# Performance work log

Hardware: AMD Instinct MI355X
Metric: run time of the kernel (lower is better)

The kernel has to match this reference:

```python
import jax, jax.numpy as jnp
import numpy as np

NUM_CODES = 1024
CODE_DIM = 256
COMMIT_W = 0.25
EPS = 1e-5
ENT_LO, ENT_HI = 0.5, 0.9
ENT_W = 0.1
VAR_FLOOR = 0.05
VAR_W = 1e-3
DECORR_W = 1e-3


def setup_inputs() -> dict:
    key = jax.random.key(0)
    k1, k2, k3 = jax.random.split(key, 3)
    inputs = jax.random.normal(k1, (16, 2048, CODE_DIM), dtype=jnp.float32)
    weight = jax.random.normal(k2, (NUM_CODES, CODE_DIM), dtype=jnp.float32) * 0.1
    usage_counts = jax.random.uniform(k3, (NUM_CODES,), dtype=jnp.float32)
    return {"inputs": inputs, "weight": weight, "usage_counts": usage_counts}


def reference(inputs, weight, usage_counts):
    K, D = weight.shape
    flat = inputs.reshape(-1, D)  # [N, D]
    # squared euclidean distances [N, K]
    dist = (flat ** 2).sum(axis=1, keepdims=True) - 2.0 * flat @ weight.T + (weight ** 2).sum(axis=1)
    idx = jnp.argmin(dist, axis=1)  # [N]
    quant = weight[idx].reshape(inputs.shape)

    commitment_loss = COMMIT_W * jnp.mean((jax.lax.stop_gradient(quant) - inputs) ** 2)
    # straight-through estimator
    quant_ste = inputs + jax.lax.stop_gradient(quant - inputs)

    # usage entropy regularizer
    probs = usage_counts + EPS
    probs = probs / jnp.maximum(probs.sum(), EPS * K)
    usage_entropy = -jnp.sum(probs * jnp.log(probs + EPS)) / np.log(float(K)).astype(np.float32)
    gap = jnp.where(usage_entropy < ENT_LO, ENT_LO - usage_entropy,
                    jnp.where(usage_entropy > ENT_HI, usage_entropy - ENT_HI, 0.0))
    entropy_loss = ENT_W * gap ** 2

    # variance floor penalty on codebook
    variance = jnp.var(weight, axis=0)
    variance_loss = VAR_W * jnp.mean(jax.nn.relu(VAR_FLOOR - variance))

    # decorrelation penalty
    wc = weight - weight.mean(axis=0, keepdims=True)
    cov = wc.T @ wc / float(K)  # [D, D]
    off_diag = cov - jnp.diag(jnp.diag(cov))
    decorrelation_loss = DECORR_W * jnp.mean(off_diag ** 2)

    total_loss = commitment_loss + entropy_loss + variance_loss + decorrelation_loss
    indices = idx.reshape(inputs.shape[:-1])
    return (quant_ste, indices, total_loss, commitment_loss, entropy_loss,
            variance_loss, decorrelation_loss, usage_entropy)
```

## Files before the change

kernel.cpp:

```cpp
#include <hip/hip_runtime.h>
#include <math.h>

#define DIMS   256
#define KCODES 1024
#define NTOT   32768
#define TAU    4.0e-4f

typedef __bf16 bf16x8 __attribute__((ext_vector_type(8)));
typedef float  f32x4  __attribute__((ext_vector_type(4)));

#define WS_COMMIT   0
#define WS_FLAGCNT  1
#define WS_DECORR   2
#define WS_COLSUM   16
#define WS_COLSQ    272
#define WS_WSQ      1024
#define WS_XSQ      2048
#define WS_FLAGS    34816
#define WS_CAND1    67584
#define WS_CAND2    329728
#define WS_CANDI    591872
#define WS_WP       854016

#define OUT_Q    0
#define OUT_IDX  8388608
#define OUT_SCAL 8421376


__global__ __launch_bounds__(256) void prep_kernel(const float* __restrict__ X,
                                                   const float* __restrict__ W,
                                                   __bf16* __restrict__ Xp,
                                                   __bf16* __restrict__ Wp2,
                                                   float* ws) {
  int b = blockIdx.x;
  int tid = threadIdx.x;
  if (b < 1056) {
    bool isW = b >= 1024;
    const float* src = isW ? W : X;
    __bf16* dst = isW ? Wp2 : Xp;
    int sqoff = isW ? WS_WSQ : WS_XSQ;
    int bb = isW ? b - 1024 : b;
    int kt = tid >> 5, mtl = (tid >> 4) & 1, lc = tid & 15;
    int row = bb * 32 + mtl * 16 + lc;
    int bt = row >> 7, c = row & 127;
    int wv = c >> 6, t = (c >> 4) & 3;
    size_t hibase = ((((size_t)(bt * 8 + kt) * 2 + wv) * 4 + t) * 2) * 512;
    const float* s = src + (size_t)row * DIMS + kt * 32;
    float sq = 0.f;
    #pragma unroll
    for (int kq = 0; kq < 4; kq++) {
      float4 u = *(const float4*)(s + kq * 8);
      float4 v = *(const float4*)(s + kq * 8 + 4);
      float f[8] = {u.x, u.y, u.z, u.w, v.x, v.y, v.z, v.w};
      bf16x8 hi, lo;
      #pragma unroll
      for (int e = 0; e < 8; e++) {
        __bf16 h = (__bf16)f[e];
        hi[e] = h;
        lo[e] = (__bf16)(f[e] - (float)h);
        sq = fmaf(f[e], f[e], sq);
      }
      size_t off = (size_t)(kq * 16 + lc) * 8;
      *(bf16x8*)&dst[hibase + off] = hi;
      *(bf16x8*)&dst[hibase + 512 + off] = lo;
    }
    atomicAdd(&ws[sqoff + row], sq);
  } else if (b < 1064) {
    int d = tid;
    int r0 = (b - 1056) * 128;
    float s = 0.f, sq = 0.f;
    #pragma unroll 8
    for (int k = 0; k < 128; k++) {
      float v = W[(size_t)(r0 + k) * DIMS + d];
      s += v;
      sq = fmaf(v, v, sq);
    }
    atomicAdd(&ws[WS_COLSUM + d], s);
    atomicAdd(&ws[WS_COLSQ + d], sq);
  } else {
    __shared__ float wi_s[2][KCODES];
    __shared__ float red2[256];
    __shared__ float mi_s[2];
    __shared__ float red[4];
    int i0 = (b - 1064) * 2;
    int rr = tid >> 1, cc = tid & 1;
    #pragma unroll
    for (int q = 0; q < 8; q++) {
      int row = q * 128 + rr;
      wi_s[cc][row] = W[(size_t)row * DIMS + i0 + cc];
    }
    __syncthreads();
    float pm = 0.f;
    #pragma unroll
    for (int q = 0; q < 8; q++) pm += wi_s[cc][rr * 8 + q];
    red2[tid] = pm;
    __syncthreads();
    if (tid < 2) {
      float s = 0.f;
      for (int k = tid; k < 256; k += 2) s += red2[k];
      mi_s[tid] = s * (1.0f / 1024.0f);
    }
    int j = tid;
    float a0 = 0.f, a1 = 0.f, sj = 0.f;
    for (int k = 0; k < KCODES; k += 4) {
      #pragma unroll
      for (int u = 0; u < 4; u++) {
        float wj = W[(size_t)(k + u) * DIMS + j];
        a0 = fmaf(wi_s[0][k + u], wj, a0);
        a1 = fmaf(wi_s[1][k + u], wj, a1);
        sj += wj;
      }
    }
    __syncthreads();
    const float inv = 1.0f / 1024.0f;
    float mj = sj * inv;
    float v = 0.f;
    float c0 = a0 * inv - mi_s[0] * mj;
    if (i0 != j) v = fmaf(c0, c0, v);
    float c1 = a1 * inv - mi_s[1] * mj;
    if (i0 + 1 != j) v = fmaf(c1, c1, v);
    #pragma unroll
    for (int m = 32; m >= 1; m >>= 1) v += __shfl_xor(v, m);
    if ((j & 63) == 0) red[j >> 6] = v;
    __syncthreads();
    if (j == 0) atomicAdd(&ws[WS_DECORR], (red[0] + red[1]) + (red[2] + red[3]));
  }
}

__global__ __launch_bounds__(256, 2) void pass1_kernel(const __bf16* __restrict__ Xp,
                                                       const __bf16* __restrict__ Wp2,
                                                       float* ws) {
  __shared__ float wsqs[128];
  __shared__ float d1L[256];
  __shared__ float d2L[256];
  __shared__ int   i1L[256];

  int tid = threadIdx.x;
  int lane = tid & 63, wave = tid >> 6;
  int wm = wave >> 1, wn = wave & 1;
  int quad = lane >> 4, col = lane & 15;
  int l = blockIdx.x;
  int bm = (l & 7) * 32 + ((l >> 3) & 31);
  int bn = l >> 8;
  int rowBase = bm * 128, cb = bn * 128;

  if (tid < 128) wsqs[tid] = ws[WS_WSQ + cb + tid];

  f32x4 acc[4][4];
  #pragma unroll
  for (int i = 0; i < 4; i++)
    #pragma unroll
    for (int j = 0; j < 4; j++) acc[i][j] = (f32x4){0.f, 0.f, 0.f, 0.f};

  const bf16x8* ab = (const bf16x8*)(Xp + (size_t)bm * 65536 + wm * 4096) + lane;
  const bf16x8* bb = (const bf16x8*)(Wp2 + (size_t)bn * 65536 + wn * 4096) + lane;

  bf16x8 Af[2][8], Bf[2][8];
  #pragma unroll
  for (int f = 0; f < 4; f++) {
    Af[0][f * 2] = ab[f * 128];
    Af[0][f * 2 + 1] = ab[f * 128 + 64];
    Bf[0][f * 2] = bb[f * 128];
    Bf[0][f * 2 + 1] = bb[f * 128 + 64];
  }
  #pragma unroll
  for (int kt = 0; kt < 8; kt++) {
    const int cur = kt & 1, nxt = cur ^ 1;
    if (kt < 7) {
      const bf16x8* an = ab + (kt + 1) * 1024;
      const bf16x8* bv = bb + (kt + 1) * 1024;
      #pragma unroll
      for (int f = 0; f < 4; f++) {
        Af[nxt][f * 2] = an[f * 128];
        Af[nxt][f * 2 + 1] = an[f * 128 + 64];
        Bf[nxt][f * 2] = bv[f * 128];
        Bf[nxt][f * 2 + 1] = bv[f * 128 + 64];
      }
    }
    #pragma unroll
    for (int nt = 0; nt < 4; nt++) {
      #pragma unroll
      for (int mt = 0; mt < 4; mt++) {
        acc[mt][nt] = __builtin_amdgcn_mfma_f32_16x16x32_bf16(Af[cur][mt * 2], Bf[cur][nt * 2], acc[mt][nt], 0, 0, 0);
        acc[mt][nt] = __builtin_amdgcn_mfma_f32_16x16x32_bf16(Af[cur][mt * 2], Bf[cur][nt * 2 + 1], acc[mt][nt], 0, 0, 0);
        acc[mt][nt] = __builtin_amdgcn_mfma_f32_16x16x32_bf16(Af[cur][mt * 2 + 1], Bf[cur][nt * 2], acc[mt][nt], 0, 0, 0);
      }
    }
  }
  __syncthreads();

  #pragma unroll
  for (int mt = 0; mt < 4; mt++) {
    #pragma unroll
    for (int r = 0; r < 4; r++) {
      float d1 = 3.0e38f, d2 = 3.0e38f;
      int i1 = 0;
      #pragma unroll
      for (int nt = 0; nt < 4; nt++) {
        int lc = wn * 64 + nt * 16 + col;
        float d = wsqs[lc] - 2.0f * acc[mt][nt][r];
        int g = cb + lc;
        if (d < d1) { d2 = d1; d1 = d; i1 = g; }
        else if (d < d2) d2 = d;
      }
      #pragma unroll
      for (int m = 1; m < 16; m <<= 1) {
        float od1 = __shfl_xor(d1, m);
        int oi1 = __shfl_xor(i1, m);
        float od2 = __shfl_xor(d2, m);
        if (od1 < d1 || (od1 == d1 && oi1 < i1)) {
          d2 = fminf(d1, fminf(d2, od2));
          d1 = od1; i1 = oi1;
        } else {
          d2 = fminf(od1, fminf(d2, od2));
        }
      }
      if (col == 0) {
        int lr = wm * 64 + mt * 16 + quad * 4 + r;
        d1L[lr * 2 + wn] = d1;
        d2L[lr * 2 + wn] = d2;
        i1L[lr * 2 + wn] = i1;
      }
    }
  }
  __syncthreads();
  if (tid < 128) {
    float a1 = d1L[tid * 2], a2 = d2L[tid * 2];
    int ai = i1L[tid * 2];
    float b1 = d1L[tid * 2 + 1], b2 = d2L[tid * 2 + 1];
    int bi = i1L[tid * 2 + 1];
    float m1, m2; int mi;
    if (b1 < a1 || (b1 == a1 && bi < ai)) { m1 = b1; mi = bi; m2 = fminf(a1, b2); }
    else { m1 = a1; mi = ai; m2 = fminf(b1, a2); }
    int o = bn * NTOT + rowBase + tid;
    ws[WS_CAND1 + o] = m1;
    ws[WS_CAND2 + o] = m2;
    ((int*)ws)[WS_CANDI + o] = mi;
  }
}

__global__ __launch_bounds__(256) void pass2_kernel(const float* __restrict__ W,
                                                    float* __restrict__ outQ,
                                                    float* __restrict__ outIdx, float* ws) {
  __shared__ int idx_s[256];
  int tid = threadIdx.x;
  int row = blockIdx.x * 256 + tid;
  const float* c1 = ws + WS_CAND1;
  const float* c2 = ws + WS_CAND2;
  const int* ci = (const int*)ws + WS_CANDI;
  float m1 = 3.0e38f, m2 = 3.0e38f;
  int mi = 0;
  #pragma unroll
  for (int b = 0; b < 8; b++) {
    int o = b * NTOT + row;
    float b1 = c1[o], b2 = c2[o];
    int bi = ci[o];
    if (b1 < m1 || (b1 == m1 && bi < mi)) { m2 = fminf(m1, b2); m1 = b1; mi = bi; }
    else { m2 = fminf(m2, b1); }
  }
  outIdx[row] = (float)mi;
  idx_s[tid] = mi;
  int* wsI = (int*)ws;
  if (m2 - m1 < TAU) {
    int p = atomicAdd(&wsI[WS_FLAGCNT], 1);
    wsI[WS_FLAGS + p] = row;
  }
  float partial = ws[WS_XSQ + row] + m1;
  #pragma unroll
  for (int m = 32; m >= 1; m >>= 1) partial += __shfl_xor(partial, m);
  if ((tid & 63) == 0) atomicAdd(&ws[WS_COMMIT], partial);
  __syncthreads();
  int wave = tid >> 6, lane = tid & 63;
  int rowBase = blockIdx.x * 256;
  #pragma unroll 4
  for (int i = 0; i < 64; i++) {
    int rl = wave * 64 + i;
    int ix = idx_s[rl];
    float4 v = ((const float4*)(W + (size_t)ix * DIMS))[lane];
    ((float4*)(outQ + (size_t)(rowBase + rl) * DIMS))[lane] = v;
  }
}

__global__ __launch_bounds__(256) void refine_kernel(const float* __restrict__ X,
                                                     const float* __restrict__ W,
                                                     float* __restrict__ outQ,
                                                     float* __restrict__ outIdx, float* ws,
                                                     const float* __restrict__ U,
                                                     float* __restrict__ out) {
  __shared__ float xs[DIMS];
  __shared__ double dm[256];
  __shared__ int im[256];
  __shared__ int chosen;
  int tid = threadIdx.x;
  if (blockIdx.x == 512) {
    __shared__ float red[256];
    float s = 0.f;
    for (int e = tid; e < KCODES; e += 256) s += U[e] + 1e-5f;
    red[tid] = s;
    __syncthreads();
    for (int st = 128; st >= 1; st >>= 1) {
      if (tid < st) red[tid] += red[tid + st];
      __syncthreads();
    }
    float S = red[0];
    __syncthreads();
    float denom = fmaxf(S, 1e-5f * 1024.0f);
    float h = 0.f;
    for (int e = tid; e < KCODES; e += 256) {
      float p = (U[e] + 1e-5f) / denom;
      h += p * logf(p + 1e-5f);
    }
    red[tid] = h;
    __syncthreads();
    for (int st = 128; st >= 1; st >>= 1) {
      if (tid < st) red[tid] += red[tid + st];
      __syncthreads();
    }
    float H = -red[0] / 6.93147180559945f;
    __syncthreads();
    float m = ws[WS_COLSUM + tid] * (1.0f / 1024.0f);
    float var = ws[WS_COLSQ + tid] * (1.0f / 1024.0f) - m * m;
    float r = 0.05f - var;
    red[tid] = r > 0.f ? r : 0.f;
    __syncthreads();
    for (int st = 128; st >= 1; st >>= 1) {
      if (tid < st) red[tid] += red[tid + st];
      __syncthreads();
    }
    if (tid == 0) {
      float varloss = 1e-3f * (red[0] / 256.0f);
      float gap = H < 0.5f ? (0.5f - H) : (H > 0.9f ? (H - 0.9f) : 0.0f);
      float entloss = 0.1f * gap * gap;
      float commit = 0.25f * ws[WS_COMMIT] / 8388608.0f;
      float dec = 1e-3f * ws[WS_DECORR] / 65536.0f;
      float* sc = out + OUT_SCAL;
      sc[0] = commit + entloss + varloss + dec;
      sc[1] = commit;
      sc[2] = entloss;
      sc[3] = varloss;
      sc[4] = dec;
      sc[5] = H;
    }
    return;
  }
  const int* wsI = (const int*)ws;
  int cnt = wsI[WS_FLAGCNT];
  const int* list = wsI + WS_FLAGS;
  for (int f = blockIdx.x; f < cnt; f += 512) {
    int row = list[f];
    __syncthreads();
    if (tid < 64) ((float4*)xs)[tid] = ((const float4*)(X + (size_t)row * DIMS))[tid];
    __syncthreads();
    double bd = 1.0e300;
    int bi = 0;
    for (int jj = 0; jj < 4; jj++) {
      int c = tid + 256 * jj;
      double a0 = 0.0, a1 = 0.0, a2 = 0.0, a3 = 0.0;
      const float* wr = W + (size_t)c * DIMS;
      #pragma unroll 4
      for (int d4 = 0; d4 < 64; d4++) {
        float4 w = ((const float4*)wr)[d4];
        float4 x = ((const float4*)xs)[d4];
        double e0 = (double)x.x - (double)w.x;
        double e1 = (double)x.y - (double)w.y;
        double e2 = (double)x.z - (double)w.z;
        double e3 = (double)x.w - (double)w.w;
        a0 += e0 * e0; a1 += e1 * e1; a2 += e2 * e2; a3 += e3 * e3;
      }
      double s = (a0 + a1) + (a2 + a3);
      if (s < bd) { bd = s; bi = c; }
    }
    dm[tid] = bd; im[tid] = bi;
    __syncthreads();
    for (int st = 128; st >= 1; st >>= 1) {
      if (tid < st) {
        if (dm[tid + st] < dm[tid] || (dm[tid + st] == dm[tid] && im[tid + st] < im[tid])) {
          dm[tid] = dm[tid + st]; im[tid] = im[tid + st];
        }
      }
      __syncthreads();
    }
    if (tid == 0) { chosen = im[0]; outIdx[row] = (float)im[0]; }
    __syncthreads();
    int ix = chosen;
    if (tid < 64)
      ((float4*)(outQ + (size_t)row * DIMS))[tid] = ((const float4*)(W + (size_t)ix * DIMS))[tid];
  }
}

extern "C" void kernel_launch(void* const* d_in, const int* in_sizes, int n_in, void* d_out,
                              int out_size, void* d_ws, size_t ws_size, hipStream_t stream) {
  const float* X = (const float*)d_in[0];
  const float* W = (const float*)d_in[1];
  const float* U = (const float*)d_in[2];
  float* out = (float*)d_out;
  float* ws = (float*)d_ws;
  __bf16* Xp = (__bf16*)(out + OUT_Q);
  __bf16* Wp2 = (__bf16*)(ws + WS_WP);

  hipMemsetAsync(d_ws, 0, 139264, stream);
  prep_kernel<<<1192, 256, 0, stream>>>(X, W, Xp, Wp2, ws);
  pass1_kernel<<<2048, 256, 0, stream>>>(Xp, Wp2, ws);
  pass2_kernel<<<NTOT / 256, 256, 0, stream>>>(W, out + OUT_Q, out + OUT_IDX, ws);
  refine_kernel<<<513, 256, 0, stream>>>(X, W, out + OUT_Q, out + OUT_IDX, ws, U, out);
}
```

Measured before the change: 237.8 us.

## Restage prep via LDS, halve pass1 N-tile, and reshape pass2 gather

The prep kernel now loads 16-row tiles into padded shared memory. From there it computes row squared norms without atomics, folds the codebook column sums into the W blocks, and writes the bf16 hi/lo packed layout with coalesced stores. This drops the separate column-sum blocks and most of the memset. Pass1 uses 64-wide code tiles with smaller accumulators, occupancy 3, and sched barriers around the MFMA block, doubling the grid and the candidate buffers to 16 per row. Pass2 reduces 16 candidates and uses 64 rows per block with a wider gather. This gives more parallelism and occupancy, but pass1 reloads the A fragments twice as often and the candidate traffic doubles.

Measured after the change: 242.6 us. +2.0%, slower.

```diff
diff --git a/kernel.cpp b/kernel.cpp
--- a/kernel.cpp
+++ b/kernel.cpp
@@ -5,6 +5,7 @@
 #define KCODES 1024
 #define NTOT   32768
 #define TAU    4.0e-4f
+#define PAD    260
 
 typedef __bf16 bf16x8 __attribute__((ext_vector_type(8)));
 typedef float  f32x4  __attribute__((ext_vector_type(4)));
@@ -18,9 +19,9 @@
 #define WS_XSQ      2048
 #define WS_FLAGS    34816
 #define WS_CAND1    67584
-#define WS_CAND2    329728
-#define WS_CANDI    591872
-#define WS_WP       854016
+#define WS_CAND2    591872
+#define WS_CANDI    1116160
+#define WS_WP       1640448
 
 #define OUT_Q    0
 #define OUT_IDX  8388608
@@ -34,55 +35,69 @@
                                                    float* ws) {
   int b = blockIdx.x;
   int tid = threadIdx.x;
-  if (b < 1056) {
-    bool isW = b >= 1024;
+  if (b < 2112) {
+    __shared__ float xs[16 * PAD];
+    bool isW = b >= 2048;
     const float* src = isW ? W : X;
     __bf16* dst = isW ? Wp2 : Xp;
-    int sqoff = isW ? WS_WSQ : WS_XSQ;
-    int bb = isW ? b - 1024 : b;
-    int kt = tid >> 5, mtl = (tid >> 4) & 1, lc = tid & 15;
-    int row = bb * 32 + mtl * 16 + lc;
-    int bt = row >> 7, c = row & 127;
-    int wv = c >> 6, t = (c >> 4) & 3;
-    size_t hibase = ((((size_t)(bt * 8 + kt) * 2 + wv) * 4 + t) * 2) * 512;
-    const float* s = src + (size_t)row * DIMS + kt * 32;
-    float sq = 0.f;
-    #pragma unroll
-    for (int kq = 0; kq < 4; kq++) {
-      float4 u = *(const float4*)(s + kq * 8);
-      float4 v = *(const float4*)(s + kq * 8 + 4);
-      float f[8] = {u.x, u.y, u.z, u.w, v.x, v.y, v.z, v.w};
+    int r0 = (isW ? (b - 2048) : b) * 16;
+    #pragma unroll
+    for (int it = 0; it < 4; it++) {
+      int t = it * 256 + tid;
+      int row = t >> 6, c4 = t & 63;
+      *(float4*)&xs[row * PAD + c4 * 4] =
+          *(const float4*)&src[(size_t)(r0 + row) * DIMS + c4 * 4];
+    }
+    __syncthreads();
+    {
+      int row = tid >> 4, q = tid & 15;
+      float sq = 0.f;
+      #pragma unroll
+      for (int e = 0; e < 16; e++) {
+        float v = xs[row * PAD + q * 16 + e];
+        sq = fmaf(v, v, sq);
+      }
+      sq += __shfl_xor(sq, 1);
+      sq += __shfl_xor(sq, 2);
+      sq += __shfl_xor(sq, 4);
+      sq += __shfl_xor(sq, 8);
+      if (q == 0) ws[(isW ? WS_WSQ : WS_XSQ) + r0 + row] = sq;
+    }
+    if (isW) {
+      float s = 0.f, sq = 0.f;
+      #pragma unroll
+      for (int row = 0; row < 16; row++) {
+        float v = xs[row * PAD + tid];
+        s += v;
+        sq = fmaf(v, v, sq);
+      }
+      atomicAdd(&ws[WS_COLSUM + tid], s);
+      atomicAdd(&ws[WS_COLSQ + tid], sq);
+    }
+    int lane = tid & 63, wave = tid >> 6;
+    int kq = lane >> 4, lc = lane & 15;
+    int bt = r0 >> 7, g = (r0 >> 4) & 7, wv = g >> 2, t = g & 3;
+    #pragma unroll
+    for (int u = 0; u < 2; u++) {
+      int kt = wave * 2 + u;
       bf16x8 hi, lo;
       #pragma unroll
       for (int e = 0; e < 8; e++) {
-        __bf16 h = (__bf16)f[e];
+        float f = xs[lc * PAD + kt * 32 + kq * 8 + e];
+        __bf16 h = (__bf16)f;
         hi[e] = h;
-        lo[e] = (__bf16)(f[e] - (float)h);
-        sq = fmaf(f[e], f[e], sq);
-      }
-      size_t off = (size_t)(kq * 16 + lc) * 8;
-      *(bf16x8*)&dst[hibase + off] = hi;
-      *(bf16x8*)&dst[hibase + 512 + off] = lo;
-    }
-    atomicAdd(&ws[sqoff + row], sq);
-  } else if (b < 1064) {
-    int d = tid;
-    int r0 = (b - 1056) * 128;
-    float s = 0.f, sq = 0.f;
-    #pragma unroll 8
-    for (int k = 0; k < 128; k++) {
-      float v = W[(size_t)(r0 + k) * DIMS + d];
-      s += v;
-      sq = fmaf(v, v, sq);
-    }
-    atomicAdd(&ws[WS_COLSUM + d], s);
-    atomicAdd(&ws[WS_COLSQ + d], sq);
+        lo[e] = (__bf16)(f - (float)h);
+      }
+      size_t base = ((((size_t)(bt * 8 + kt) * 2 + wv) * 4 + t) * 2) * 512;
+      *(bf16x8*)&dst[base + lane * 8] = hi;
+      *(bf16x8*)&dst[base + 512 + lane * 8] = lo;
+    }
   } else {
     __shared__ float wi_s[2][KCODES];
     __shared__ float red2[256];
     __shared__ float mi_s[2];
     __shared__ float red[4];
-    int i0 = (b - 1064) * 2;
+    int i0 = (b - 2112) * 2;
     int rr = tid >> 1, cc = tid & 1;
     #pragma unroll
     for (int q = 0; q < 8; q++) {
@@ -127,10 +142,10 @@
   }
 }
 
-__global__ __launch_bounds__(256, 2) void pass1_kernel(const __bf16* __restrict__ Xp,
+__global__ __launch_bounds__(256, 3) void pass1_kernel(const __bf16* __restrict__ Xp,
                                                        const __bf16* __restrict__ Wp2,
                                                        float* ws) {
-  __shared__ float wsqs[128];
+  __shared__ float wsqs[64];
   __shared__ float d1L[256];
   __shared__ float d2L[256];
   __shared__ int   i1L[256];
@@ -142,26 +157,29 @@
   int l = blockIdx.x;
   int bm = (l & 7) * 32 + ((l >> 3) & 31);
   int bn = l >> 8;
-  int rowBase = bm * 128, cb = bn * 128;
-
-  if (tid < 128) wsqs[tid] = ws[WS_WSQ + cb + tid];
-
-  f32x4 acc[4][4];
+  int rowBase = bm * 128, cb = bn * 64;
+
+  if (tid < 64) wsqs[tid] = ws[WS_WSQ + cb + tid];
+
+  f32x4 acc[4][2];
   #pragma unroll
   for (int i = 0; i < 4; i++)
     #pragma unroll
-    for (int j = 0; j < 4; j++) acc[i][j] = (f32x4){0.f, 0.f, 0.f, 0.f};
-
-  const bf16x8* ab = (const bf16x8*)(Xp + (size_t)bm * 65536 + wm * 4096) + lane;
-  const bf16x8* bb = (const bf16x8*)(Wp2 + (size_t)bn * 65536 + wn * 4096) + lane;
-
-  bf16x8 Af[2][8], Bf[2][8];
-  #pragma unroll
-  for (int f = 0; f < 4; f++) {
-    Af[0][f * 2] = ab[f * 128];
-    Af[0][f * 2 + 1] = ab[f * 128 + 64];
-    Bf[0][f * 2] = bb[f * 128];
-    Bf[0][f * 2 + 1] = bb[f * 128 + 64];
+    for (int j = 0; j < 2; j++) acc[i][j] = (f32x4){0.f, 0.f, 0.f, 0.f};
+
+  const bf16x8* ab = (const bf16x8*)Xp + (size_t)bm * 8192 + wm * 512 + lane;
+  const bf16x8* bb = (const bf16x8*)Wp2 + (size_t)(bn >> 1) * 8192 + (bn & 1) * 512 + wn * 256 + lane;
+
+  bf16x8 Af[2][8], Bf[2][4];
+  #pragma unroll
+  for (int mt = 0; mt < 4; mt++) {
+    Af[0][mt * 2] = ab[mt * 128];
+    Af[0][mt * 2 + 1] = ab[mt * 128 + 64];
+  }
+  #pragma unroll
+  for (int nt = 0; nt < 2; nt++) {
+    Bf[0][nt * 2] = bb[nt * 128];
+    Bf[0][nt * 2 + 1] = bb[nt * 128 + 64];
   }
   #pragma unroll
   for (int kt = 0; kt < 8; kt++) {
@@ -170,15 +188,19 @@
       const bf16x8* an = ab + (kt + 1) * 1024;
       const bf16x8* bv = bb + (kt + 1) * 1024;
       #pragma unroll
-      for (int f = 0; f < 4; f++) {
-        Af[nxt][f * 2] = an[f * 128];
-        Af[nxt][f * 2 + 1] = an[f * 128 + 64];
-        Bf[nxt][f * 2] = bv[f * 128];
-        Bf[nxt][f * 2 + 1] = bv[f * 128 + 64];
-      }
-    }
-    #pragma unroll
-    for (int nt = 0; nt < 4; nt++) {
+      for (int mt = 0; mt < 4; mt++) {
+        Af[nxt][mt * 2] = an[mt * 128];
+        Af[nxt][mt * 2 + 1] = an[mt * 128 + 64];
+      }
+      #pragma unroll
+      for (int nt = 0; nt < 2; nt++) {
+        Bf[nxt][nt * 2] = bv[nt * 128];
+        Bf[nxt][nt * 2 + 1] = bv[nt * 128 + 64];
+      }
+    }
+    __builtin_amdgcn_sched_barrier(0);
+    #pragma unroll
+    for (int nt = 0; nt < 2; nt++) {
       #pragma unroll
       for (int mt = 0; mt < 4; mt++) {
         acc[mt][nt] = __builtin_amdgcn_mfma_f32_16x16x32_bf16(Af[cur][mt * 2], Bf[cur][nt * 2], acc[mt][nt], 0, 0, 0);
@@ -186,6 +208,7 @@
         acc[mt][nt] = __builtin_amdgcn_mfma_f32_16x16x32_bf16(Af[cur][mt * 2 + 1], Bf[cur][nt * 2], acc[mt][nt], 0, 0, 0);
       }
     }
+    __builtin_amdgcn_sched_barrier(0);
   }
   __syncthreads();
 
@@ -196,8 +219,8 @@
       float d1 = 3.0e38f, d2 = 3.0e38f;
       int i1 = 0;
       #pragma unroll
-      for (int nt = 0; nt < 4; nt++) {
-        int lc = wn * 64 + nt * 16 + col;
+      for (int nt = 0; nt < 2; nt++) {
+        int lc = wn * 32 + nt * 16 + col;
         float d = wsqs[lc] - 2.0f * acc[mt][nt][r];
         int g = cb + lc;
         if (d < d1) { d2 = d1; d1 = d; i1 = g; }
@@ -242,42 +265,46 @@
 __global__ __launch_bounds__(256) void pass2_kernel(const float* __restrict__ W,
                                                     float* __restrict__ outQ,
                                                     float* __restrict__ outIdx, float* ws) {
-  __shared__ int idx_s[256];
+  __shared__ int idx_s[64];
   int tid = threadIdx.x;
-  int row = blockIdx.x * 256 + tid;
-  const float* c1 = ws + WS_CAND1;
-  const float* c2 = ws + WS_CAND2;
-  const int* ci = (const int*)ws + WS_CANDI;
-  float m1 = 3.0e38f, m2 = 3.0e38f;
-  int mi = 0;
-  #pragma unroll
-  for (int b = 0; b < 8; b++) {
-    int o = b * NTOT + row;
-    float b1 = c1[o], b2 = c2[o];
-    int bi = ci[o];
-    if (b1 < m1 || (b1 == m1 && bi < mi)) { m2 = fminf(m1, b2); m1 = b1; mi = bi; }
-    else { m2 = fminf(m2, b1); }
-  }
-  outIdx[row] = (float)mi;
-  idx_s[tid] = mi;
-  int* wsI = (int*)ws;
-  if (m2 - m1 < TAU) {
-    int p = atomicAdd(&wsI[WS_FLAGCNT], 1);
-    wsI[WS_FLAGS + p] = row;
-  }
-  float partial = ws[WS_XSQ + row] + m1;
-  #pragma unroll
-  for (int m = 32; m >= 1; m >>= 1) partial += __shfl_xor(partial, m);
-  if ((tid & 63) == 0) atomicAdd(&ws[WS_COMMIT], partial);
+  int rowBase = blockIdx.x * 64;
+  if (tid < 64) {
+    int row = rowBase + tid;
+    const float* c1 = ws + WS_CAND1;
+    const float* c2 = ws + WS_CAND2;
+    const int* ci = (const int*)ws + WS_CANDI;
+    float m1 = 3.0e38f, m2 = 3.0e38f;
+    int mi = 0;
+    #pragma unroll
+    for (int b = 0; b < 16; b++) {
+      int o = b * NTOT + row;
+      float b1 = c1[o], b2 = c2[o];
+      int bi = ci[o];
+      if (b1 < m1 || (b1 == m1 && bi < mi)) { m2 = fminf(m1, b2); m1 = b1; mi = bi; }
+      else { m2 = fminf(m2, b1); }
+    }
+    outIdx[row] = (float)mi;
+    idx_s[tid] = mi;
+    int* wsI = (int*)ws;
+    if (m2 - m1 < TAU) {
+      int p = atomicAdd(&wsI[WS_FLAGCNT], 1);
+      wsI[WS_FLAGS + p] = row;
+    }
+    float partial = ws[WS_XSQ + row] + m1;
+    #pragma unroll
+    for (int m = 32; m >= 1; m >>= 1) partial += __shfl_xor(partial, m);
+    if (tid == 0) atomicAdd(&ws[WS_COMMIT], partial);
+  }
   __syncthreads();
-  int wave = tid >> 6, lane = tid & 63;
-  int rowBase = blockIdx.x * 256;
-  #pragma unroll 4
-  for (int i = 0; i < 64; i++) {
-    int rl = wave * 64 + i;
+  int r = tid >> 4, l16 = tid & 15;
+  #pragma unroll
+  for (int it = 0; it < 4; it++) {
+    int rl = it * 16 + r;
     int ix = idx_s[rl];
-    float4 v = ((const float4*)(W + (size_t)ix * DIMS))[lane];
-    ((float4*)(outQ + (size_t)(rowBase + rl) * DIMS))[lane] = v;
+    const float4* wsrc = (const float4*)(W + (size_t)ix * DIMS);
+    float4* qdst = (float4*)(outQ + (size_t)(rowBase + rl) * DIMS);
+    #pragma unroll
+    for (int c = 0; c < 4; c++) qdst[c * 16 + l16] = wsrc[c * 16 + l16];
   }
 }
 
@@ -398,9 +425,9 @@
   __bf16* Xp = (__bf16*)(out + OUT_Q);
   __bf16* Wp2 = (__bf16*)(ws + WS_WP);
 
-  hipMemsetAsync(d_ws, 0, 139264, stream);
-  prep_kernel<<<1192, 256, 0, stream>>>(X, W, Xp, Wp2, ws);
-  pass1_kernel<<<2048, 256, 0, stream>>>(Xp, Wp2, ws);
-  pass2_kernel<<<NTOT / 256, 256, 0, stream>>>(W, out + OUT_Q, out + OUT_IDX, ws);
+  hipMemsetAsync(d_ws, 0, 2112, stream);
+  prep_kernel<<<2240, 256, 0, stream>>>(X, W, Xp, Wp2, ws);
+  pass1_kernel<<<4096, 256, 0, stream>>>(Xp, Wp2, ws);
+  pass2_kernel<<<512, 256, 0, stream>>>(W, out + OUT_Q, out + OUT_IDX, ws);
   refine_kernel<<<513, 256, 0, stream>>>(X, W, out + OUT_Q, out + OUT_IDX, ws, U, out);
 }
```
